# Kernel optimization log

Hardware: AMD Instinct MI355X
Metric: run time of the kernel (lower is better)

## Reference

```python
import jax, jax.numpy as jnp
import numpy as np

N_NODES = 100_000
N_EDGES = 3_200_000
N_FEAT = 500
HIDDEN = 64
N_CLASSES = 40
N_LAYERS = 8
ALPHA = 0.1
THETA = 0.5


def setup_inputs() -> dict:
    key = jax.random.key(0)
    ks = jax.random.split(key, 9)
    x = jax.random.normal(ks[0], (N_NODES, N_FEAT), dtype=jnp.float32)
    edge_src = jax.random.randint(ks[1], (N_EDGES,), 0, N_NODES, dtype=jnp.int32)
    edge_dst = jax.random.randint(ks[2], (N_EDGES,), 0, N_NODES, dtype=jnp.int32)
    # adj_t is assumed pre-normalized (normalize=False); scale ~ 1/avg_degree
    edge_weight = jax.random.uniform(ks[3], (N_EDGES,), dtype=jnp.float32) / 32.0
    lin0_w = jax.random.normal(ks[4], (N_FEAT, HIDDEN), dtype=jnp.float32) / np.float32(np.sqrt(N_FEAT))
    lin0_b = jnp.zeros((HIDDEN,), dtype=jnp.float32)
    conv_w = jax.random.normal(ks[5], (N_LAYERS, HIDDEN, HIDDEN), dtype=jnp.float32) / np.float32(np.sqrt(HIDDEN))
    lin1_w = jax.random.normal(ks[6], (HIDDEN, N_CLASSES), dtype=jnp.float32) / np.float32(np.sqrt(HIDDEN))
    lin1_b = jnp.zeros((N_CLASSES,), dtype=jnp.float32)
    return {"x": x, "edge_src": edge_src, "edge_dst": edge_dst, "edge_weight": edge_weight,
            "lin0_w": lin0_w, "lin0_b": lin0_b, "conv_w": conv_w, "lin1_w": lin1_w, "lin1_b": lin1_b}


def _spmm(edge_src, edge_dst, edge_weight, h):
    # out[i] = sum_{e: dst[e]==i} w[e] * h[src[e]]  (adj_t @ h)
    msgs = edge_weight[:, None] * h[edge_src]  # [E, H]
    return jax.ops.segment_sum(msgs, edge_dst, num_segments=h.shape[0])


def reference(x, edge_src, edge_dst, edge_weight, lin0_w, lin0_b, conv_w, lin1_w, lin1_b):
    h = jax.nn.relu(x @ lin0_w + lin0_b)  # [N, H]
    x0 = h
    for l in range(N_LAYERS):
        agg = _spmm(edge_src, edge_dst, edge_weight, h)
        z = (1.0 - ALPHA) * agg + ALPHA * x0  # initial-residual blend
        beta = np.float32(np.log(THETA / (l + 1) + 1.0))  # identity-mapping coeff
        h = jax.nn.relu((1.0 - beta) * z + beta * (z @ conv_w[l]))
    out = h @ lin1_w + lin1_b  # [N, C]
    return jax.nn.log_softmax(out, axis=-1)
```

## Files before the change

### kernel.cpp

```cpp
#include <hip/hip_runtime.h>
#include <math.h>

#define NNODES 100000
#define NEDGES 3200000
#define NFEAT  500
#define HID    64
#define NCLS   40
#define NLAYERS 8
#define NPB    16
#define NODES_PER_PART 12500

typedef __attribute__((ext_vector_type(8))) short short8;
typedef __attribute__((ext_vector_type(4))) float floatx4;

static __device__ __forceinline__ float b2f(unsigned short u) {
    return __uint_as_float(((unsigned)u) << 16);
}
static __device__ __forceinline__ unsigned short f2b(float f) {
    unsigned u = __float_as_uint(f);
    return (unsigned short)((u + 0x7FFFu + ((u >> 16) & 1u)) >> 16);
}
static __device__ __forceinline__ ushort4 pk4(float4 v) {
    return make_ushort4(f2b(v.x), f2b(v.y), f2b(v.z), f2b(v.w));
}

__global__ __launch_bounds__(256) void lin0_kernel(const float* __restrict__ x,
    const float* __restrict__ w, const float* __restrict__ b,
    unsigned short* __restrict__ h0)
{
    __shared__ unsigned short as_[128][40];
    __shared__ unsigned short wt[64][40];
    const int tid = threadIdx.x;
    const int wv = tid >> 6, lane = tid & 63;
    const int ln15 = lane & 15, q = lane >> 4;
    const int m0 = blockIdx.x * 128;

    floatx4 acc[2][4];
#pragma unroll
    for (int i = 0; i < 2; ++i)
#pragma unroll
        for (int t = 0; t < 4; ++t) acc[i][t] = (floatx4){0.f, 0.f, 0.f, 0.f};

    const int r_ = tid >> 1, hh = tid & 1;
    int gms = m0 + r_; if (gms >= NNODES) gms = NNODES - 1;
    const float* xrow = x + (size_t)gms * NFEAT;

    for (int c = 0; c < 16; ++c) {
        const int k0 = c * 32;
        {
            float4 v0, v1, v2, v3;
            if (c < 15 || hh == 0) {
                const float4* p4 = (const float4*)(xrow + k0 + 16 * hh);
                v0 = p4[0]; v1 = p4[1]; v2 = p4[2]; v3 = p4[3];
            } else {
                v0 = *(const float4*)(xrow + 496);
                v1 = make_float4(0, 0, 0, 0); v2 = v1; v3 = v1;
            }
            ushort4* dst4 = (ushort4*)&as_[r_][16 * hh];
            dst4[0] = pk4(v0); dst4[1] = pk4(v1); dst4[2] = pk4(v2); dst4[3] = pk4(v3);
        }
#pragma unroll
        for (int ii = 0; ii < 2; ++ii) {
            int i = tid + ii * 256;
            int k = i >> 4, nb = (i & 15) * 4;
            float4 v = make_float4(0, 0, 0, 0);
            if (c < 15 || i < 320)
                v = ((const float4*)(w + (size_t)k0 * HID))[i];
            wt[nb + 0][k] = f2b(v.x); wt[nb + 1][k] = f2b(v.y);
            wt[nb + 2][k] = f2b(v.z); wt[nb + 3][k] = f2b(v.w);
        }
        __syncthreads();
        short8 af[2], bfr[4];
#pragma unroll
        for (int mt = 0; mt < 2; ++mt)
            af[mt] = *(const short8*)&as_[32 * wv + 16 * mt + ln15][8 * q];
#pragma unroll
        for (int t = 0; t < 4; ++t)
            bfr[t] = *(const short8*)&wt[16 * t + ln15][8 * q];
#pragma unroll
        for (int mt = 0; mt < 2; ++mt)
#pragma unroll
            for (int t = 0; t < 4; ++t)
                acc[mt][t] = __builtin_amdgcn_mfma_f32_16x16x32_bf16(
                    af[mt], bfr[t], acc[mt][t], 0, 0, 0);
        __syncthreads();
    }
    float bv[4];
#pragma unroll
    for (int t = 0; t < 4; ++t) bv[t] = b[16 * t + ln15];
#pragma unroll
    for (int mt = 0; mt < 2; ++mt)
#pragma unroll
        for (int r = 0; r < 4; ++r) {
            int gm = m0 + 32 * wv + 16 * mt + q * 4 + r;
            if (gm < NNODES) {
#pragma unroll
                for (int t = 0; t < 4; ++t)
                    h0[(size_t)gm * HID + 16 * t + ln15] =
                        f2b(fmaxf(acc[mt][t][r] + bv[t], 0.f));
            }
        }
}

__global__ __launch_bounds__(256) void count_kernel(const int* __restrict__ dst,
                                                    int* __restrict__ deg)
{
    const int part = blockIdx.x & 7;
    const int e = (blockIdx.x >> 3) * 256 + threadIdx.x;
    const int d = dst[e];
    if (d / NODES_PER_PART == part) atomicAdd(&deg[d], 1);
}

__global__ __launch_bounds__(1024) void chunk_sum_kernel(const int* __restrict__ deg,
                                                         int* __restrict__ csum)
{
    __shared__ int s[1024];
    int i = blockIdx.x * 1024 + threadIdx.x;
    s[threadIdx.x] = (i < NNODES) ? ((deg[i] + 3) & ~3) : 0;
    __syncthreads();
    for (int off = 512; off > 0; off >>= 1) {
        if (threadIdx.x < off) s[threadIdx.x] += s[threadIdx.x + off];
        __syncthreads();
    }
    if (threadIdx.x == 0) csum[blockIdx.x] = s[0];
}

__global__ __launch_bounds__(128) void chunk_base_kernel(const int* __restrict__ csum,
    int* __restrict__ cbase, int* __restrict__ offs, int nchunks)
{
    __shared__ int s[128];
    const int t = threadIdx.x;
    int v = (t < nchunks) ? csum[t] : 0;
    s[t] = v;
    __syncthreads();
    for (int off = 1; off < 128; off <<= 1) {
        int u = (t >= off) ? s[t - off] : 0;
        __syncthreads();
        s[t] += u;
        __syncthreads();
    }
    if (t < nchunks) cbase[t] = s[t] - v;
    if (t == nchunks - 1) offs[NNODES] = s[t];
}

__global__ __launch_bounds__(1024) void scan_kernel(const int* __restrict__ deg,
    const int* __restrict__ cbase, int* __restrict__ offs, int* __restrict__ cursor)
{
    __shared__ int s[1024];
    int i = blockIdx.x * 1024 + threadIdx.x;
    int v = (i < NNODES) ? ((deg[i] + 3) & ~3) : 0;
    s[threadIdx.x] = v;
    __syncthreads();
    for (int off = 1; off < 1024; off <<= 1) {
        int t = (threadIdx.x >= off) ? s[threadIdx.x - off] : 0;
        __syncthreads();
        s[threadIdx.x] += t;
        __syncthreads();
    }
    if (i < NNODES) {
        int excl = cbase[blockIdx.x] + s[threadIdx.x] - v;
        offs[i] = excl;
        cursor[i] = excl;
    }
}

__global__ __launch_bounds__(256) void scatter_kernel(const int* __restrict__ src,
    const int* __restrict__ dst, const float* __restrict__ w,
    int* __restrict__ cursor, int2* __restrict__ srcw)
{
    const int part = blockIdx.x & 7;
    const int e = (blockIdx.x >> 3) * 256 + threadIdx.x;
    const int d = dst[e];
    if (d / NODES_PER_PART == part) {
        int pos = atomicAdd(&cursor[d], 1);
        srcw[pos] = make_int2(src[e] * 128, __float_as_int(w[e]));
    }
}

__global__ __launch_bounds__(256) void pad_kernel(const int* __restrict__ offs,
    const int* __restrict__ deg, int2* __restrict__ srcw)
{
    int n = blockIdx.x * 256 + threadIdx.x;
    if (n < NNODES) {
        int e = offs[n] + deg[n], e1 = offs[n + 1];
        for (; e < e1; ++e) srcw[e] = make_int2(0, 0);
    }
}

__global__ __launch_bounds__(256) void spmm_layer_kernel(
    const unsigned short* __restrict__ h_in, const unsigned short* __restrict__ x0,
    unsigned short* __restrict__ h_out, const int* __restrict__ offs,
    const int2* __restrict__ srcw, const float* __restrict__ Wg, float beta)
{
    __shared__ float          zs [NPB][72];
    __shared__ unsigned short zsb[NPB][72];
    __shared__ unsigned short WbT[HID][72];
    const int tid = threadIdx.x;

    for (int i = tid; i < 1024; i += 256) {
        float4 v = ((const float4*)Wg)[i];
        int k = i >> 4, j = (i & 15) * 4;
        WbT[j + 0][k] = f2b(v.x); WbT[j + 1][k] = f2b(v.y);
        WbT[j + 2][k] = f2b(v.z); WbT[j + 3][k] = f2b(v.w);
    }

    const int wv = tid >> 6, lane = tid & 63;
    const int qt = lane >> 4, ln = lane & 15;
    const int nloc = wv * 4 + qt;
    const int n = blockIdx.x * NPB + nloc;
    int e = offs[n];
    const int e1 = offs[n + 1];
    const char* hbl = (const char*)h_in + ln * 8;
    float a0 = 0.f, a1 = 0.f, a2 = 0.f, a3 = 0.f;
#pragma unroll 2
    for (; e < e1; e += 2) {
        int4 pr = *(const int4*)(srcw + e);
        uint2 v0 = *(const uint2*)(hbl + pr.x);
        uint2 v1 = *(const uint2*)(hbl + pr.z);
        float w0 = __int_as_float(pr.y), w1 = __int_as_float(pr.w);
        a0 = fmaf(w0, __uint_as_float(v0.x << 16), a0);
        a1 = fmaf(w0, __uint_as_float(v0.x & 0xffff0000u), a1);
        a2 = fmaf(w0, __uint_as_float(v0.y << 16), a2);
        a3 = fmaf(w0, __uint_as_float(v0.y & 0xffff0000u), a3);
        a0 = fmaf(w1, __uint_as_float(v1.x << 16), a0);
        a1 = fmaf(w1, __uint_as_float(v1.x & 0xffff0000u), a1);
        a2 = fmaf(w1, __uint_as_float(v1.y << 16), a2);
        a3 = fmaf(w1, __uint_as_float(v1.y & 0xffff0000u), a3);
    }
    uint2 xv = *(const uint2*)((const char*)x0 + (size_t)n * 128 + ln * 8);
    float z0 = 0.9f * a0 + 0.1f * __uint_as_float(xv.x << 16);
    float z1 = 0.9f * a1 + 0.1f * __uint_as_float(xv.x & 0xffff0000u);
    float z2 = 0.9f * a2 + 0.1f * __uint_as_float(xv.y << 16);
    float z3 = 0.9f * a3 + 0.1f * __uint_as_float(xv.y & 0xffff0000u);
    *(float4*)&zs[nloc][4 * ln] = make_float4(z0, z1, z2, z3);
    *(ushort4*)&zsb[nloc][4 * ln] = make_ushort4(f2b(z0), f2b(z1), f2b(z2), f2b(z3));
    __syncthreads();

    floatx4 acc = (floatx4){0.f, 0.f, 0.f, 0.f};
#pragma unroll
    for (int s = 0; s < 2; ++s) {
        short8 af = *(const short8*)&zsb[ln][32 * s + 8 * qt];
        short8 bf = *(const short8*)&WbT[16 * wv + ln][32 * s + 8 * qt];
        acc = __builtin_amdgcn_mfma_f32_16x16x32_bf16(af, bf, acc, 0, 0, 0);
    }
    const float ob = 1.f - beta;
    const size_t base = (size_t)blockIdx.x * NPB;
#pragma unroll
    for (int r4 = 0; r4 < 4; ++r4) {
        const int node = qt * 4 + r4;
        const int j = 16 * wv + ln;
        float hv = fmaxf(ob * zs[node][j] + beta * acc[r4], 0.f);
        h_out[(base + node) * HID + j] = f2b(hv);
    }
}

__global__ __launch_bounds__(256) void final_kernel(const unsigned short* __restrict__ h,
    const float* __restrict__ w1, const float* __restrict__ b1, float* __restrict__ out)
{
    const int m = threadIdx.x >> 6, j = threadIdx.x & 63;
    const long n = (long)blockIdx.x * 4 + m;
    const int jj = (j < NCLS) ? j : NCLS - 1;
    const ushort4* hrow = (const ushort4*)(h + n * HID);
    float acc = b1[jj];
#pragma unroll
    for (int k4 = 0; k4 < 16; ++k4) {
        ushort4 hv = hrow[k4];
        const int k = k4 * 4;
        acc = fmaf(b2f(hv.x), w1[(k + 0) * NCLS + jj], acc);
        acc = fmaf(b2f(hv.y), w1[(k + 1) * NCLS + jj], acc);
        acc = fmaf(b2f(hv.z), w1[(k + 2) * NCLS + jj], acc);
        acc = fmaf(b2f(hv.w), w1[(k + 3) * NCLS + jj], acc);
    }
    float lg = (j < NCLS) ? acc : -INFINITY;
    float mx = lg;
#pragma unroll
    for (int o = 32; o > 0; o >>= 1) mx = fmaxf(mx, __shfl_xor(mx, o, 64));
    float ex = (j < NCLS) ? expf(acc - mx) : 0.f;
    float sm = ex;
#pragma unroll
    for (int o = 32; o > 0; o >>= 1) sm += __shfl_xor(sm, o, 64);
    if (j < NCLS) out[n * NCLS + j] = acc - mx - logf(sm);
}

extern "C" void kernel_launch(void* const* d_in, const int* in_sizes, int n_in,
                              void* d_out, int out_size, void* d_ws, size_t ws_size,
                              hipStream_t stream)
{
    const float* x    = (const float*)d_in[0];
    const int*   esrc = (const int*)d_in[1];
    const int*   edst = (const int*)d_in[2];
    const float* ew   = (const float*)d_in[3];
    const float* l0w  = (const float*)d_in[4];
    const float* l0b  = (const float*)d_in[5];
    const float* cw   = (const float*)d_in[6];
    const float* l1w  = (const float*)d_in[7];
    const float* l1b  = (const float*)d_in[8];
    float* out = (float*)d_out;

    char* p = (char*)d_ws;
    unsigned short* h0 = (unsigned short*)p; p += (size_t)NNODES * HID * 2;
    unsigned short* hA = (unsigned short*)p; p += (size_t)NNODES * HID * 2;
    unsigned short* hB = (unsigned short*)p; p += (size_t)NNODES * HID * 2;
    int2*  srcw = (int2*)p;  p += ((size_t)NEDGES + 4 * NNODES) * 8;
    int* offs   = (int*)p;   p += (size_t)(NNODES + 1) * 4;
    int* cursor = (int*)p;   p += (size_t)NNODES * 4;
    int* deg    = (int*)p;   p += (size_t)NNODES * 4;
    int* csum   = (int*)p;   p += 512;
    int* cbase  = (int*)p;   p += 512;

    const int nchunks = (NNODES + 1023) / 1024;

    hipMemsetAsync(deg, 0, NNODES * sizeof(int), stream);
    lin0_kernel<<<(NNODES + 127) / 128, 256, 0, stream>>>(x, l0w, l0b, h0);
    count_kernel<<<(NEDGES / 256) * 8, 256, 0, stream>>>(edst, deg);
    chunk_sum_kernel<<<nchunks, 1024, 0, stream>>>(deg, csum);
    chunk_base_kernel<<<1, 128, 0, stream>>>(csum, cbase, offs, nchunks);
    scan_kernel<<<nchunks, 1024, 0, stream>>>(deg, cbase, offs, cursor);
    scatter_kernel<<<(NEDGES / 256) * 8, 256, 0, stream>>>(esrc, edst, ew, cursor, srcw);
    pad_kernel<<<(NNODES + 255) / 256, 256, 0, stream>>>(offs, deg, srcw);

    const unsigned short* hin = h0;
    unsigned short* bufs[2] = { hA, hB };
    for (int l = 0; l < NLAYERS; ++l) {
        float beta = (float)log(0.5 / (double)(l + 1) + 1.0);
        unsigned short* hout = bufs[l & 1];
        spmm_layer_kernel<<<NNODES / NPB, 256, 0, stream>>>(
            hin, h0, hout, offs, srcw, cw + (size_t)l * HID * HID, beta);
        hin = hout;
    }
    final_kernel<<<NNODES / 4, 256, 0, stream>>>(hin, l1w, l1b, out);
}
```

Measured before the change: 1.181 ms.

## Bucket CSR edges by source range and unroll SpMM gather to four edges

The CSR build now counts and scatters edges into per-destination sub-buckets keyed by source-node range (16 buckets). This makes each row's neighbours roughly sorted by source, so the per-layer gathers get better cache locality. The count and scatter kernels drop the 8-way destination-partitioned multi-pass launch and run a single pass, with atomics spread across 16x more counters. The degree and cursor arrays reuse the hA/hB feature buffers as scratch. The SpMM inner loop now processes four edges per iteration to expose more independent loads, which relies on rows being padded to multiples of four.

```diff
diff --git a/kernel.cpp b/kernel.cpp
--- a/kernel.cpp
+++ b/kernel.cpp
@@ -8,7 +8,8 @@
 #define NCLS   40
 #define NLAYERS 8
 #define NPB    16
-#define NODES_PER_PART 12500
+#define NBUCK  16
+#define NODES_PER_BUCK 6250
 
 typedef __attribute__((ext_vector_type(8))) short short8;
 typedef __attribute__((ext_vector_type(4))) float floatx4;
@@ -102,27 +103,34 @@
         }
 }
 
-__global__ __launch_bounds__(256) void count_kernel(const int* __restrict__ dst,
-                                                    int* __restrict__ deg)
-{
-    const int part = blockIdx.x & 7;
-    const int e = (blockIdx.x >> 3) * 256 + threadIdx.x;
-    const int d = dst[e];
-    if (d / NODES_PER_PART == part) atomicAdd(&deg[d], 1);
-}
-
-__global__ __launch_bounds__(1024) void chunk_sum_kernel(const int* __restrict__ deg,
+__global__ __launch_bounds__(256) void count_kernel(const int* __restrict__ src,
+    const int* __restrict__ dst, int* __restrict__ degb)
+{
+    const int e = blockIdx.x * 256 + threadIdx.x;
+    const int d = dst[e], s = src[e];
+    atomicAdd(&degb[d * NBUCK + s / NODES_PER_BUCK], 1);
+}
+
+__global__ __launch_bounds__(1024) void chunk_sum_kernel(const int* __restrict__ degb,
                                                          int* __restrict__ csum)
 {
-    __shared__ int s[1024];
+    __shared__ int sm[1024];
     int i = blockIdx.x * 1024 + threadIdx.x;
-    s[threadIdx.x] = (i < NNODES) ? ((deg[i] + 3) & ~3) : 0;
+    int v = 0;
+    if (i < NNODES) {
+        const int4* q = (const int4*)(degb + (size_t)i * NBUCK);
+        int4 a = q[0], b = q[1], c = q[2], d = q[3];
+        v = a.x + a.y + a.z + a.w + b.x + b.y + b.z + b.w
+          + c.x + c.y + c.z + c.w + d.x + d.y + d.z + d.w;
+        v = (v + 3) & ~3;
+    }
+    sm[threadIdx.x] = v;
     __syncthreads();
     for (int off = 512; off > 0; off >>= 1) {
-        if (threadIdx.x < off) s[threadIdx.x] += s[threadIdx.x + off];
-        __syncthreads();
-    }
-    if (threadIdx.x == 0) csum[blockIdx.x] = s[0];
+        if (threadIdx.x < off) sm[threadIdx.x] += sm[threadIdx.x + off];
+        __syncthreads();
+    }
+    if (threadIdx.x == 0) csum[blockIdx.x] = sm[0];
 }
 
 __global__ __launch_bounds__(128) void chunk_base_kernel(const int* __restrict__ csum,
@@ -143,46 +151,61 @@
     if (t == nchunks - 1) offs[NNODES] = s[t];
 }
 
-__global__ __launch_bounds__(1024) void scan_kernel(const int* __restrict__ deg,
-    const int* __restrict__ cbase, int* __restrict__ offs, int* __restrict__ cursor)
-{
-    __shared__ int s[1024];
+__global__ __launch_bounds__(1024) void scan_kernel(const int* __restrict__ degb,
+    const int* __restrict__ cbase, int* __restrict__ offs, int* __restrict__ cur)
+{
+    __shared__ int sm[1024];
     int i = blockIdx.x * 1024 + threadIdx.x;
-    int v = (i < NNODES) ? ((deg[i] + 3) & ~3) : 0;
-    s[threadIdx.x] = v;
+    int dv[16];
+    int v = 0;
+    if (i < NNODES) {
+        const int4* q = (const int4*)(degb + (size_t)i * NBUCK);
+#pragma unroll
+        for (int j = 0; j < 4; ++j) {
+            int4 a = q[j];
+            dv[4 * j + 0] = a.x; dv[4 * j + 1] = a.y;
+            dv[4 * j + 2] = a.z; dv[4 * j + 3] = a.w;
+            v += a.x + a.y + a.z + a.w;
+        }
+        v = (v + 3) & ~3;
+    }
+    sm[threadIdx.x] = v;
     __syncthreads();
     for (int off = 1; off < 1024; off <<= 1) {
-        int t = (threadIdx.x >= off) ? s[threadIdx.x - off] : 0;
-        __syncthreads();
-        s[threadIdx.x] += t;
+        int t = (threadIdx.x >= off) ? sm[threadIdx.x - off] : 0;
+        __syncthreads();
+        sm[threadIdx.x] += t;
         __syncthreads();
     }
     if (i < NNODES) {
-        int excl = cbase[blockIdx.x] + s[threadIdx.x] - v;
+        int excl = cbase[blockIdx.x] + sm[threadIdx.x] - v;
         offs[i] = excl;
-        cursor[i] = excl;
+        int run = excl;
+#pragma unroll
+        for (int b = 0; b < NBUCK; ++b) {
+            cur[(size_t)i * NBUCK + b] = run;
+            run += dv[b];
+        }
     }
 }
 
 __global__ __launch_bounds__(256) void scatter_kernel(const int* __restrict__ src,
     const int* __restrict__ dst, const float* __restrict__ w,
-    int* __restrict__ cursor, int2* __restrict__ srcw)
-{
-    const int part = blockIdx.x & 7;
-    const int e = (blockIdx.x >> 3) * 256 + threadIdx.x;
-    const int d = dst[e];
-    if (d / NODES_PER_PART == part) {
-        int pos = atomicAdd(&cursor[d], 1);
-        srcw[pos] = make_int2(src[e] * 128, __float_as_int(w[e]));
-    }
+    int* __restrict__ cur, int2* __restrict__ srcw)
+{
+    const int e = blockIdx.x * 256 + threadIdx.x;
+    const int d = dst[e], s = src[e];
+    int pos = atomicAdd(&cur[d * NBUCK + s / NODES_PER_BUCK], 1);
+    srcw[pos] = make_int2(s * 128, __float_as_int(w[e]));
 }
 
 __global__ __launch_bounds__(256) void pad_kernel(const int* __restrict__ offs,
-    const int* __restrict__ deg, int2* __restrict__ srcw)
+    const int* __restrict__ cur, int2* __restrict__ srcw)
 {
     int n = blockIdx.x * 256 + threadIdx.x;
     if (n < NNODES) {
-        int e = offs[n] + deg[n], e1 = offs[n + 1];
+        int e = cur[(size_t)n * NBUCK + NBUCK - 1];
+        int e1 = offs[n + 1];
         for (; e < e1; ++e) srcw[e] = make_int2(0, 0);
     }
 }
@@ -212,12 +235,15 @@
     const int e1 = offs[n + 1];
     const char* hbl = (const char*)h_in + ln * 8;
     float a0 = 0.f, a1 = 0.f, a2 = 0.f, a3 = 0.f;
-#pragma unroll 2
-    for (; e < e1; e += 2) {
-        int4 pr = *(const int4*)(srcw + e);
-        uint2 v0 = *(const uint2*)(hbl + pr.x);
-        uint2 v1 = *(const uint2*)(hbl + pr.z);
-        float w0 = __int_as_float(pr.y), w1 = __int_as_float(pr.w);
+    for (; e < e1; e += 4) {
+        int4 p0 = *(const int4*)(srcw + e);
+        int4 p1 = *(const int4*)(srcw + e + 2);
+        uint2 v0 = *(const uint2*)(hbl + p0.x);
+        uint2 v1 = *(const uint2*)(hbl + p0.z);
+        uint2 v2 = *(const uint2*)(hbl + p1.x);
+        uint2 v3 = *(const uint2*)(hbl + p1.z);
+        float w0 = __int_as_float(p0.y), w1 = __int_as_float(p0.w);
+        float w2 = __int_as_float(p1.y), w3 = __int_as_float(p1.w);
         a0 = fmaf(w0, __uint_as_float(v0.x << 16), a0);
         a1 = fmaf(w0, __uint_as_float(v0.x & 0xffff0000u), a1);
         a2 = fmaf(w0, __uint_as_float(v0.y << 16), a2);
@@ -226,6 +252,14 @@
         a1 = fmaf(w1, __uint_as_float(v1.x & 0xffff0000u), a1);
         a2 = fmaf(w1, __uint_as_float(v1.y << 16), a2);
         a3 = fmaf(w1, __uint_as_float(v1.y & 0xffff0000u), a3);
+        a0 = fmaf(w2, __uint_as_float(v2.x << 16), a0);
+        a1 = fmaf(w2, __uint_as_float(v2.x & 0xffff0000u), a1);
+        a2 = fmaf(w2, __uint_as_float(v2.y << 16), a2);
+        a3 = fmaf(w2, __uint_as_float(v2.y & 0xffff0000u), a3);
+        a0 = fmaf(w3, __uint_as_float(v3.x << 16), a0);
+        a1 = fmaf(w3, __uint_as_float(v3.x & 0xffff0000u), a1);
+        a2 = fmaf(w3, __uint_as_float(v3.y << 16), a2);
+        a3 = fmaf(w3, __uint_as_float(v3.y & 0xffff0000u), a3);
     }
     uint2 xv = *(const uint2*)((const char*)x0 + (size_t)n * 128 + ln * 8);
     float z0 = 0.9f * a0 + 0.1f * __uint_as_float(xv.x << 16);
@@ -303,21 +337,21 @@
     unsigned short* hB = (unsigned short*)p; p += (size_t)NNODES * HID * 2;
     int2*  srcw = (int2*)p;  p += ((size_t)NEDGES + 4 * NNODES) * 8;
     int* offs   = (int*)p;   p += (size_t)(NNODES + 1) * 4;
-    int* cursor = (int*)p;   p += (size_t)NNODES * 4;
-    int* deg    = (int*)p;   p += (size_t)NNODES * 4;
     int* csum   = (int*)p;   p += 512;
     int* cbase  = (int*)p;   p += 512;
+    int* degb = (int*)hB;
+    int* cur  = (int*)hA;
 
     const int nchunks = (NNODES + 1023) / 1024;
 
-    hipMemsetAsync(deg, 0, NNODES * sizeof(int), stream);
+    hipMemsetAsync(degb, 0, (size_t)NNODES * NBUCK * sizeof(int), stream);
     lin0_kernel<<<(NNODES + 127) / 128, 256, 0, stream>>>(x, l0w, l0b, h0);
-    count_kernel<<<(NEDGES / 256) * 8, 256, 0, stream>>>(edst, deg);
-    chunk_sum_kernel<<<nchunks, 1024, 0, stream>>>(deg, csum);
+    count_kernel<<<NEDGES / 256, 256, 0, stream>>>(esrc, edst, degb);
+    chunk_sum_kernel<<<nchunks, 1024, 0, stream>>>(degb, csum);
     chunk_base_kernel<<<1, 128, 0, stream>>>(csum, cbase, offs, nchunks);
-    scan_kernel<<<nchunks, 1024, 0, stream>>>(deg, cbase, offs, cursor);
-    scatter_kernel<<<(NEDGES / 256) * 8, 256, 0, stream>>>(esrc, edst, ew, cursor, srcw);
-    pad_kernel<<<(NNODES + 255) / 256, 256, 0, stream>>>(offs, deg, srcw);
+    scan_kernel<<<nchunks, 1024, 0, stream>>>(degb, cbase, offs, cur);
+    scatter_kernel<<<NEDGES / 256, 256, 0, stream>>>(esrc, edst, ew, cur, srcw);
+    pad_kernel<<<(NNODES + 255) / 256, 256, 0, stream>>>(offs, cur, srcw);
 
     const unsigned short* hin = h0;
     unsigned short* bufs[2] = { hA, hB };
```

Result: slower. 1.257 ms (+6.4%).
